# Kernel tuning notes

Hardware: AMD Instinct MI355X
Metric: run time of the kernel (lower is better)

Reference implementation:

```python
import jax, jax.numpy as jnp
import numpy as np
from jax import lax

VDECAY = 0.5
VTH = 0.5
GRAD_WIN = 0.5

B, IN_DIM, T = 128, 2048, 32
H = 2048
OUT = 512

@jax.custom_vjp
def spike(v):
    return (v > VTH).astype(v.dtype)

def _spike_fwd(v):
    return spike(v), v

def _spike_bwd(v, g):
    # rectangular surrogate gradient (PseudoSpikeRect)
    return (g * (jnp.abs(v - VTH) < GRAD_WIN).astype(g.dtype),)

spike.defvjp(_spike_fwd, _spike_bwd)

def setup_inputs() -> dict:
    key = jax.random.key(0)
    ks = jax.random.split(key, 4)
    scale = 1.0 / np.sqrt(2048)
    return {
        "spike_data": (jax.random.uniform(ks[0], (B, IN_DIM, T)) < 0.3).astype(jnp.float32),
        "h0_volt": jnp.zeros((B, H), jnp.float32),
        "h0_spike": jnp.zeros((B, H), jnp.float32),
        "h1_volt": jnp.zeros((B, H), jnp.float32),
        "h1_spike": jnp.zeros((B, H), jnp.float32),
        "o_volt": jnp.zeros((B, OUT), jnp.float32),
        "o_spike": jnp.zeros((B, OUT), jnp.float32),
        "W0": jax.random.normal(ks[1], (H, IN_DIM), jnp.float32) * scale,
        "b0": jnp.zeros((H,), jnp.float32),
        "W1": jax.random.normal(ks[2], (H, H), jnp.float32) * scale,
        "b1": jnp.zeros((H,), jnp.float32),
        "Wo": jax.random.normal(ks[3], (OUT, H), jnp.float32) * scale,
        "bo": jnp.zeros((OUT,), jnp.float32),
        "batch_size": B,
        "spike_ts": T,
    }

def _lif(x, volt, spk, W, b):
    # volt decays only where no spike occurred (soft reset via (1 - spike))
    volt = VDECAY * volt * (1.0 - spk) + x @ W.T + b
    new_spk = spike(volt)
    return new_spk, volt

def reference(spike_data, h0_volt, h0_spike, h1_volt, h1_spike, o_volt, o_spike,
              W0, b0, W1, b1, Wo, bo, batch_size, spike_ts):
    x = spike_data.reshape(batch_size, -1, spike_ts)
    xt = jnp.transpose(x, (2, 0, 1))  # [T, B, in_dim]

    def step(carry, inp):
        (v0, s0), (v1, s1), (vo, so) = carry
        s0, v0 = _lif(inp, v0, s0, W0, b0)
        s1, v1 = _lif(s0, v1, s1, W1, b1)
        so, vo = _lif(s1, vo, so, Wo, bo)
        return ((v0, s0), (v1, s1), (vo, so)), so

    carry0 = ((h0_volt, h0_spike), (h1_volt, h1_spike), (o_volt, o_spike))
    _, out_spikes = lax.scan(step, carry0, xt)  # [T, B, OUT]
    return out_spikes.sum(axis=0)
```

## Files before the change

### kernel.cpp

```cpp
#include <hip/hip_runtime.h>
#include <cstdint>

#define B_   128
#define T_   32
#define IN_  2048
#define H_   2048
#define OUT_ 512

typedef __attribute__((address_space(1))) const void* gas_cp;
typedef __attribute__((address_space(3))) void* las_p;

__global__ __launch_bounds__(256) void k_transpose(const float* __restrict__ in,
                                                   float* __restrict__ Xt) {
    int idx = blockIdx.x * 256 + threadIdx.x;
    int b = idx >> 11;
    int i = idx & (IN_ - 1);
    const float4* p = (const float4*)(in + (size_t)idx * T_);
#pragma unroll
    for (int q = 0; q < 8; ++q) {
        float4 v = p[q];
        int t = q * 4;
        Xt[((size_t)((t + 0) * B_ + b) << 11) + i] = v.x;
        Xt[((size_t)((t + 1) * B_ + b) << 11) + i] = v.y;
        Xt[((size_t)((t + 2) * B_ + b) << 11) + i] = v.z;
        Xt[((size_t)((t + 3) * B_ + b) << 11) + i] = v.w;
    }
}

__global__ __launch_bounds__(256, 2)
void k_gemm_128(const float* __restrict__ A, const float* __restrict__ W,
                float* __restrict__ C, int M, int N, int K) {
    constexpr int BM = 128, BN = 128, BK = 32;
    constexpr int BUFF = (BM + BN) * BK;
    __shared__ alignas(16) float lds[2][BUFF];

    const int tid = threadIdx.x;
    const int tx  = tid & 15;
    const int ty  = tid >> 4;
    const int m0  = blockIdx.y * BM;
    const int n0  = blockIdx.x * BN;
    const int w   = tid >> 6;

    const float* srcA[4];
    const float* srcW[4];
    int dstA[4], dstW[4];
#pragma unroll
    for (int q = 0; q < 4; ++q) {
        int L = q * 256 + tid;
        int r = L >> 3;
        int s = ((L & 7) - ((r + (r >> 4)) & 7)) & 7;
        srcA[q] = A + (size_t)(m0 + r) * K + s * 4;
        srcW[q] = W + (size_t)(n0 + r) * K + s * 4;
        dstA[q] = q * 1024 + w * 256;
        dstW[q] = BM * BK + q * 1024 + w * 256;
    }

    float acc[8][8];
    float tot[8][8];
#pragma unroll
    for (int i = 0; i < 8; ++i)
#pragma unroll
        for (int j = 0; j < 8; ++j) { acc[i][j] = 0.0f; tot[i][j] = 0.0f; }

    const int nkt = K / BK;

#pragma unroll
    for (int q = 0; q < 4; ++q) {
        __builtin_amdgcn_global_load_lds((gas_cp)srcA[q], (las_p)&lds[0][dstA[q]], 16, 0, 0);
        srcA[q] += BK;
    }
#pragma unroll
    for (int q = 0; q < 4; ++q) {
        __builtin_amdgcn_global_load_lds((gas_cp)srcW[q], (las_p)&lds[0][dstW[q]], 16, 0, 0);
        srcW[q] += BK;
    }

    int cur = 0;
    for (int kt = 0; kt < nkt; ++kt) {
        __syncthreads();

        if (kt + 1 < nkt) {
            int nb = cur ^ 1;
#pragma unroll
            for (int q = 0; q < 4; ++q) {
                __builtin_amdgcn_global_load_lds((gas_cp)srcA[q], (las_p)&lds[nb][dstA[q]], 16, 0, 0);
                srcA[q] += BK;
            }
#pragma unroll
            for (int q = 0; q < 4; ++q) {
                __builtin_amdgcn_global_load_lds((gas_cp)srcW[q], (las_p)&lds[nb][dstW[q]], 16, 0, 0);
                srcW[q] += BK;
            }
        }

        const float* At = &lds[cur][0];
        const float* Wt = &lds[cur][BM * BK];

#pragma unroll
        for (int gk = 0; gk < 8; ++gk) {
            float4 av[8], wv[8];
#pragma unroll
            for (int i = 0; i < 8; ++i) {
                int r = ty + 16 * i;
                int rot = (r + (r >> 4)) & 7;
                av[i] = *(const float4*)&At[r * BK + (((gk + rot) & 7) << 2)];
            }
#pragma unroll
            for (int j = 0; j < 8; ++j) {
                int r = tx + 16 * j;
                int rot = (r + (r >> 4)) & 7;
                wv[j] = *(const float4*)&Wt[r * BK + (((gk + rot) & 7) << 2)];
            }
#pragma unroll
            for (int q = 0; q < 4; ++q)
#pragma unroll
                for (int i = 0; i < 8; ++i)
#pragma unroll
                    for (int j = 0; j < 8; ++j)
                        acc[i][j] = __builtin_fmaf(((const float*)&av[i])[q],
                                                   ((const float*)&wv[j])[q],
                                                   acc[i][j]);
        }

        if (((kt + 1) & 15) == 0) {
#pragma unroll
            for (int i = 0; i < 8; ++i)
#pragma unroll
                for (int j = 0; j < 8; ++j) {
                    tot[i][j] = tot[i][j] + acc[i][j];
                    acc[i][j] = 0.0f;
                }
        }
        cur ^= 1;
    }

#pragma unroll
    for (int i = 0; i < 8; ++i)
#pragma unroll
        for (int j = 0; j < 8; ++j)
            C[(size_t)(m0 + ty + 16 * i) * N + (n0 + tx + 16 * j)] = tot[i][j];
}

__global__ __launch_bounds__(256)
void k_gemm_seq(const float* __restrict__ A, const float* __restrict__ W,
                float* __restrict__ C, int M, int N, int K) {
    constexpr int BM = 64, BN = 128, BK = 32;
    constexpr int NT = 8;
    constexpr int BUFF = (BM + BN) * BK;
    __shared__ alignas(16) float lds[2][BUFF];

    const int tid = threadIdx.x;
    const int tx  = tid & 15;
    const int ty  = tid >> 4;
    const int m0  = blockIdx.y * BM;
    const int n0  = blockIdx.x * BN;
    const int w   = tid >> 6;

    const float* srcA[2];
    int dstA[2];
#pragma unroll
    for (int q = 0; q < 2; ++q) {
        int L = q * 256 + tid;
        int r = L >> 3;
        int s = ((L & 7) - ((r + (r >> 4)) & 7)) & 7;
        srcA[q] = A + (size_t)(m0 + r) * K + s * 4;
        dstA[q] = q * 1024 + w * 256;
    }
    const float* srcW[4];
    int dstW[4];
#pragma unroll
    for (int q = 0; q < 4; ++q) {
        int L = q * 256 + tid;
        int r = L >> 3;
        int s = ((L & 7) - ((r + (r >> 4)) & 7)) & 7;
        srcW[q] = W + (size_t)(n0 + r) * K + s * 4;
        dstW[q] = BM * BK + q * 1024 + w * 256;
    }

    float acc[4][NT];
    float tot[4][NT];
#pragma unroll
    for (int i = 0; i < 4; ++i)
#pragma unroll
        for (int j = 0; j < NT; ++j) { acc[i][j] = 0.0f; tot[i][j] = 0.0f; }

    const int nkt = K / BK;

#pragma unroll
    for (int q = 0; q < 2; ++q) {
        __builtin_amdgcn_global_load_lds((gas_cp)srcA[q], (las_p)&lds[0][dstA[q]], 16, 0, 0);
        srcA[q] += BK;
    }
#pragma unroll
    for (int q = 0; q < 4; ++q) {
        __builtin_amdgcn_global_load_lds((gas_cp)srcW[q], (las_p)&lds[0][dstW[q]], 16, 0, 0);
        srcW[q] += BK;
    }

    int cur = 0;
    for (int kt = 0; kt < nkt; ++kt) {
        __syncthreads();

        if (kt + 1 < nkt) {
            int nb = cur ^ 1;
#pragma unroll
            for (int q = 0; q < 2; ++q) {
                __builtin_amdgcn_global_load_lds((gas_cp)srcA[q], (las_p)&lds[nb][dstA[q]], 16, 0, 0);
                srcA[q] += BK;
            }
#pragma unroll
            for (int q = 0; q < 4; ++q) {
                __builtin_amdgcn_global_load_lds((gas_cp)srcW[q], (las_p)&lds[nb][dstW[q]], 16, 0, 0);
                srcW[q] += BK;
            }
        }

        const float* At = &lds[cur][0];
        const float* Wt = &lds[cur][BM * BK];

#pragma unroll
        for (int gk = 0; gk < 8; ++gk) {
            float4 av[4], wv[NT];
#pragma unroll
            for (int i = 0; i < 4; ++i) {
                int r = ty + 16 * i;
                int rot = (r + (r >> 4)) & 7;
                av[i] = *(const float4*)&At[r * BK + (((gk + rot) & 7) << 2)];
            }
#pragma unroll
            for (int j = 0; j < NT; ++j) {
                int r = tx + 16 * j;
                int rot = (r + (r >> 4)) & 7;
                wv[j] = *(const float4*)&Wt[r * BK + (((gk + rot) & 7) << 2)];
            }
#pragma unroll
            for (int q = 0; q < 4; ++q)
#pragma unroll
                for (int i = 0; i < 4; ++i)
#pragma unroll
                    for (int j = 0; j < NT; ++j)
                        acc[i][j] = __builtin_fmaf(((const float*)&av[i])[q],
                                                   ((const float*)&wv[j])[q],
                                                   acc[i][j]);
        }

        if (((kt + 1) & 15) == 0) {
#pragma unroll
            for (int i = 0; i < 4; ++i)
#pragma unroll
                for (int j = 0; j < NT; ++j) {
                    tot[i][j] = tot[i][j] + acc[i][j];
                    acc[i][j] = 0.0f;
                }
        }
        cur ^= 1;
    }

#pragma unroll
    for (int i = 0; i < 4; ++i)
#pragma unroll
        for (int j = 0; j < NT; ++j)
            C[(size_t)(m0 + ty + 16 * i) * N + (n0 + tx + 16 * j)] = tot[i][j];
}

__global__ __launch_bounds__(256) void k_scan_h(const float* __restrict__ Acc,
                                                const float* __restrict__ v_init,
                                                const float* __restrict__ s_init,
                                                const float* __restrict__ bias,
                                                float* __restrict__ Sout) {
    int idx = blockIdx.x * 256 + threadIdx.x;
    int h = idx & (H_ - 1);
    float v = v_init[idx];
    float s = s_init[idx];
    float bb = bias[h];
#pragma unroll
    for (int t = 0; t < T_; ++t) {
        float x = Acc[(size_t)t * (B_ * H_) + idx];
        float d = 0.5f * v;
        d = d * (1.0f - s);
        v = d + x;
        v = v + bb;
        s = (v > 0.5f) ? 1.0f : 0.0f;
        Sout[(size_t)t * (B_ * H_) + idx] = s;
    }
}

__global__ __launch_bounds__(256) void k_scan_o(const float* __restrict__ Acc,
                                                const float* __restrict__ v_init,
                                                const float* __restrict__ s_init,
                                                const float* __restrict__ bias,
                                                float* __restrict__ out) {
    int idx = blockIdx.x * 256 + threadIdx.x;
    int o = idx & (OUT_ - 1);
    float v = v_init[idx];
    float s = s_init[idx];
    float bb = bias[o];
    float acc = 0.0f;
#pragma unroll
    for (int t = 0; t < T_; ++t) {
        float x = Acc[(size_t)t * (B_ * OUT_) + idx];
        float d = 0.5f * v;
        d = d * (1.0f - s);
        v = d + x;
        v = v + bb;
        s = (v > 0.5f) ? 1.0f : 0.0f;
        acc += s;
    }
    out[idx] = acc;
}


extern "C" void kernel_launch(void* const* d_in, const int* in_sizes, int n_in,
                              void* d_out, int out_size, void* d_ws, size_t ws_size,
                              hipStream_t stream) {
    const float* spike_data = (const float*)d_in[0];
    const float* h0_volt  = (const float*)d_in[1];
    const float* h0_spike = (const float*)d_in[2];
    const float* h1_volt  = (const float*)d_in[3];
    const float* h1_spike = (const float*)d_in[4];
    const float* o_volt   = (const float*)d_in[5];
    const float* o_spike  = (const float*)d_in[6];
    const float* W0 = (const float*)d_in[7];
    const float* b0 = (const float*)d_in[8];
    const float* W1 = (const float*)d_in[9];
    const float* b1 = (const float*)d_in[10];
    const float* Wo = (const float*)d_in[11];
    const float* bo = (const float*)d_in[12];
    float* out = (float*)d_out;

    char* ws = (char*)d_ws;
    const size_t MB = (size_t)1 << 20;
    float* Xt = (float*)(ws);
    float* S0 = (float*)(ws + 32 * MB);
    float* Ab = (float*)(ws + 64 * MB);
    float* S1 = Xt;

    const int M = T_ * B_;

    k_transpose<<<(B_ * IN_) / 256, 256, 0, stream>>>(spike_data, Xt);

    k_gemm_128<<<dim3(H_ / 128, M / 128), 256, 0, stream>>>(Xt, W0, Ab, M, H_, IN_);
    k_scan_h<<<(B_ * H_) / 256, 256, 0, stream>>>(Ab, h0_volt, h0_spike, b0, S0);

    k_gemm_128<<<dim3(H_ / 128, M / 128), 256, 0, stream>>>(S0, W1, Ab, M, H_, H_);
    k_scan_h<<<(B_ * H_) / 256, 256, 0, stream>>>(Ab, h1_volt, h1_spike, b1, S1);

    k_gemm_seq<<<dim3(OUT_ / 128, M / 64), 256, 0, stream>>>(S1, Wo, Ab, M, OUT_, H_);
    k_scan_o<<<(B_ * OUT_) / 256, 256, 0, stream>>>(Ab, o_volt, o_spike, bo, out);

    (void)in_sizes; (void)n_in; (void)out_size; (void)ws_size;
}
```

Measured before the change: 1.495 ms.

## Software-pipeline LDS reads in 128x128 GEMM with XOR swizzle and unrolled k-tiles

Rewrites the k_gemm_128 inner loop to double-buffer W fragments in registers across k-substeps, so LDS reads for the next step overlap with FMAs of the current one. The rotation-based swizzle becomes an XOR swizzle with precomputed byte offsets, which removes per-iteration address arithmetic. The k loop is unrolled two tiles at a time with fixed buffer indices, and the W source pointers are derived from A plus a single delta to save registers. Occupancy hints move from a minimum of 2 blocks to waves_per_eu(1,2), and the K dimension is hardcoded to 64 tiles, which assumes K=2048.

```diff
diff --git a/kernel.cpp b/kernel.cpp
--- a/kernel.cpp
+++ b/kernel.cpp
@@ -1,5 +1,6 @@
 #include <hip/hip_runtime.h>
 #include <cstdint>
+#include <cstddef>
 
 #define B_   128
 #define T_   32
@@ -27,12 +28,14 @@
     }
 }
 
-__global__ __launch_bounds__(256, 2)
+__global__ __launch_bounds__(256)
+__attribute__((amdgpu_waves_per_eu(1, 2)))
 void k_gemm_128(const float* __restrict__ A, const float* __restrict__ W,
                 float* __restrict__ C, int M, int N, int K) {
     constexpr int BM = 128, BN = 128, BK = 32;
     constexpr int BUFF = (BM + BN) * BK;
     __shared__ alignas(16) float lds[2][BUFF];
+    float* lds_f = &lds[0][0];
 
     const int tid = threadIdx.x;
     const int tx  = tid & 15;
@@ -42,18 +45,29 @@
     const int w   = tid >> 6;
 
     const float* srcA[4];
-    const float* srcW[4];
     int dstA[4], dstW[4];
 #pragma unroll
     for (int q = 0; q < 4; ++q) {
         int L = q * 256 + tid;
         int r = L >> 3;
-        int s = ((L & 7) - ((r + (r >> 4)) & 7)) & 7;
+        int s = (L & 7) ^ ((r + (r >> 4)) & 7);
         srcA[q] = A + (size_t)(m0 + r) * K + s * 4;
-        srcW[q] = W + (size_t)(n0 + r) * K + s * 4;
         dstA[q] = q * 1024 + w * 256;
         dstW[q] = BM * BK + q * 1024 + w * 256;
     }
+    const ptrdiff_t wdel = (W - A) + (ptrdiff_t)(n0 - m0) * K;
+
+    int offA[8], offW[8];
+#pragma unroll
+    for (int i = 0; i < 8; ++i) {
+        int r = ty + 16 * i;
+        offA[i] = r * 128 + (((r + (r >> 4)) & 7) << 4);
+    }
+#pragma unroll
+    for (int j = 0; j < 8; ++j) {
+        int r = tx + 16 * j;
+        offW[j] = BM * BK * 4 + r * 128 + (((r + (r >> 4)) & 7) << 4);
+    }
 
     float acc[8][8];
     float tot[8][8];
@@ -62,67 +76,74 @@
 #pragma unroll
         for (int j = 0; j < 8; ++j) { acc[i][j] = 0.0f; tot[i][j] = 0.0f; }
 
-    const int nkt = K / BK;
-
-#pragma unroll
-    for (int q = 0; q < 4; ++q) {
-        __builtin_amdgcn_global_load_lds((gas_cp)srcA[q], (las_p)&lds[0][dstA[q]], 16, 0, 0);
-        srcA[q] += BK;
-    }
-#pragma unroll
-    for (int q = 0; q < 4; ++q) {
-        __builtin_amdgcn_global_load_lds((gas_cp)srcW[q], (las_p)&lds[0][dstW[q]], 16, 0, 0);
-        srcW[q] += BK;
-    }
-
-    int cur = 0;
-    for (int kt = 0; kt < nkt; ++kt) {
-        __syncthreads();
-
-        if (kt + 1 < nkt) {
-            int nb = cur ^ 1;
-#pragma unroll
-            for (int q = 0; q < 4; ++q) {
-                __builtin_amdgcn_global_load_lds((gas_cp)srcA[q], (las_p)&lds[nb][dstA[q]], 16, 0, 0);
-                srcA[q] += BK;
-            }
-#pragma unroll
-            for (int q = 0; q < 4; ++q) {
-                __builtin_amdgcn_global_load_lds((gas_cp)srcW[q], (las_p)&lds[nb][dstW[q]], 16, 0, 0);
-                srcW[q] += BK;
-            }
-        }
-
-        const float* At = &lds[cur][0];
-        const float* Wt = &lds[cur][BM * BK];
-
-#pragma unroll
-        for (int gk = 0; gk < 8; ++gk) {
-            float4 av[8], wv[8];
-#pragma unroll
-            for (int i = 0; i < 8; ++i) {
-                int r = ty + 16 * i;
-                int rot = (r + (r >> 4)) & 7;
-                av[i] = *(const float4*)&At[r * BK + (((gk + rot) & 7) << 2)];
-            }
-#pragma unroll
-            for (int j = 0; j < 8; ++j) {
-                int r = tx + 16 * j;
-                int rot = (r + (r >> 4)) & 7;
-                wv[j] = *(const float4*)&Wt[r * BK + (((gk + rot) & 7) << 2)];
-            }
-#pragma unroll
-            for (int q = 0; q < 4; ++q)
-#pragma unroll
-                for (int i = 0; i < 8; ++i)
-#pragma unroll
-                    for (int j = 0; j < 8; ++j)
-                        acc[i][j] = __builtin_fmaf(((const float*)&av[i])[q],
-                                                   ((const float*)&wv[j])[q],
-                                                   acc[i][j]);
-        }
-
-        if (((kt + 1) & 15) == 0) {
+#define RD4(BB, OFF) (*(const float4*)((const char*)lds_f + (BB) * 32768 + (OFF)))
+
+#define PREFETCH(NB)                                                        \
+    {                                                                       \
+        _Pragma("unroll")                                                   \
+        for (int q = 0; q < 4; ++q) {                                       \
+            __builtin_amdgcn_global_load_lds((gas_cp)srcA[q],               \
+                (las_p)&lds_f[(NB) * BUFF + dstA[q]], 16, 0, 0);            \
+            __builtin_amdgcn_global_load_lds((gas_cp)(srcA[q] + wdel),      \
+                (las_p)&lds_f[(NB) * BUFF + dstW[q]], 16, 0, 0);            \
+            srcA[q] += BK;                                                  \
+        }                                                                   \
+    }
+
+#define GKSTEP(BB, GKC, WC, WN, LOADN)                                      \
+    {                                                                       \
+        float4 av[4];                                                       \
+        _Pragma("unroll")                                                   \
+        for (int i = 0; i < 4; ++i) av[i] = RD4(BB, offA[i] ^ (GKC));       \
+        if (LOADN) {                                                        \
+            _Pragma("unroll")                                               \
+            for (int j = 0; j < 8; ++j) WN[j] = RD4(BB, offW[j] ^ ((GKC) + 16)); \
+        }                                                                   \
+        _Pragma("unroll")                                                   \
+        for (int q = 0; q < 4; ++q)                                         \
+            _Pragma("unroll")                                               \
+            for (int i = 0; i < 4; ++i)                                     \
+                _Pragma("unroll")                                           \
+                for (int j = 0; j < 8; ++j)                                 \
+                    acc[i][j] = __builtin_fmaf(((const float*)&av[i])[q],   \
+                                               ((const float*)&WC[j])[q],   \
+                                               acc[i][j]);                  \
+        _Pragma("unroll")                                                   \
+        for (int i = 0; i < 4; ++i) av[i] = RD4(BB, offA[4 + i] ^ (GKC));   \
+        _Pragma("unroll")                                                   \
+        for (int q = 0; q < 4; ++q)                                         \
+            _Pragma("unroll")                                               \
+            for (int i = 0; i < 4; ++i)                                     \
+                _Pragma("unroll")                                           \
+                for (int j = 0; j < 8; ++j)                                 \
+                    acc[4 + i][j] = __builtin_fmaf(((const float*)&av[i])[q], \
+                                                   ((const float*)&WC[j])[q], \
+                                                   acc[4 + i][j]);          \
+    }
+
+#define KTILE(BB, DO_PF, NB)                                                \
+    {                                                                       \
+        __syncthreads();                                                    \
+        if (DO_PF) PREFETCH(NB);                                            \
+        float4 wvA[8], wvB[8];                                              \
+        _Pragma("unroll")                                                   \
+        for (int j = 0; j < 8; ++j) wvA[j] = RD4(BB, offW[j]);              \
+        GKSTEP(BB, 0,   wvA, wvB, 1)                                        \
+        GKSTEP(BB, 16,  wvB, wvA, 1)                                        \
+        GKSTEP(BB, 32,  wvA, wvB, 1)                                        \
+        GKSTEP(BB, 48,  wvB, wvA, 1)                                        \
+        GKSTEP(BB, 64,  wvA, wvB, 1)                                        \
+        GKSTEP(BB, 80,  wvB, wvA, 1)                                        \
+        GKSTEP(BB, 96,  wvA, wvB, 1)                                        \
+        GKSTEP(BB, 112, wvB, wvA, 0)                                        \
+    }
+
+    PREFETCH(0);
+
+    for (int kt = 0; kt < 64; kt += 2) {
+        KTILE(0, 1, 1)
+        KTILE(1, (kt < 62), 0)
+        if (((kt + 2) & 15) == 0) {
 #pragma unroll
             for (int i = 0; i < 8; ++i)
 #pragma unroll
@@ -131,7 +152,6 @@
                     acc[i][j] = 0.0f;
                 }
         }
-        cur ^= 1;
     }
 
 #pragma unroll
@@ -139,6 +159,11 @@
 #pragma unroll
         for (int j = 0; j < 8; ++j)
             C[(size_t)(m0 + ty + 16 * i) * N + (n0 + tx + 16 * j)] = tot[i][j];
+
+#undef KTILE
+#undef GKSTEP
+#undef PREFETCH
+#undef RD4
 }
 
 __global__ __launch_bounds__(256)
```

After: 5.241 ms. 3.51x slower.
